# Kernel tuning notes

Measured on AMD Instinct MI355X. Metric: run time of the kernel, lower is better.

The kernel has to match this reference:

```python
import jax, jax.numpy as jnp
import numpy as np

EPS = 1e-05

def _rmsnorm(h, w, eps=EPS):
    var = jnp.mean(h * h, axis=-1, keepdims=True)
    return h * jax.lax.rsqrt(var + eps) * w

def setup_inputs() -> dict:
    key = jax.random.key(0)
    ks = jax.random.split(key, 9)
    B, S, H, I, R = 2, 4096, 4096, 14336, 1592
    s_h = 1.0 / np.sqrt(H)
    s_r = 1.0 / np.sqrt(R)
    s_i = 1.0 / np.sqrt(I)
    return {
        "x": jax.random.normal(ks[0], (B, S, H), jnp.float32),
        "residual": jax.random.normal(ks[1], (B, S, H), jnp.float32),
        "ln_w": jnp.ones((H,), jnp.float32),
        "w_gate_v": jax.random.normal(ks[2], (H, R), jnp.float32) * s_h,
        "w_gate_u": jax.random.normal(ks[3], (R, I), jnp.float32) * s_r,
        "w_up_v": jax.random.normal(ks[4], (H, R), jnp.float32) * s_h,
        "w_up_u": jax.random.normal(ks[5], (R, I), jnp.float32) * s_r,
        "w_down_v": jax.random.normal(ks[6], (I, R), jnp.float32) * s_i,
        "w_down_u": jax.random.normal(ks[7], (R, H), jnp.float32) * s_r,
    }

def reference(x, residual, ln_w, w_gate_v, w_gate_u, w_up_v, w_up_u, w_down_v, w_down_u):
    # fused residual add + RMSNorm (as in the fused NKI kernel path)
    h = x + residual                    # [B,S,H]
    n = _rmsnorm(h, ln_w)               # [B,S,H]
    # low-rank gate / up projections: H -> R -> I
    gate = jax.nn.silu(jnp.einsum('bsh,hr,ri->bsi', n, w_gate_v, w_gate_u))
    up = jnp.einsum('bsh,hr,ri->bsi', n, w_up_v, w_up_u)
    # low-rank down projection: I -> R -> H
    out = jnp.einsum('bsi,ir,rh->bsh', gate * up, w_down_v, w_down_u)
    return out
```

## Files before the change

### kernel.cpp

```cpp
#include <hip/hip_runtime.h>
#include <cstdint>
#include <cstddef>

typedef __attribute__((ext_vector_type(8))) short short8;
typedef __attribute__((ext_vector_type(4))) float floatx4;

__device__ __forceinline__ float bf2f(unsigned short u) {
    union { float f; uint32_t i; } v; v.i = ((uint32_t)u) << 16; return v.f;
}
__device__ __forceinline__ unsigned short f2bf(float f) {
    union { float f; uint32_t i; } v; v.f = f;
    uint32_t r = v.i + 0x7FFFu + ((v.i >> 16) & 1u);
    return (unsigned short)(r >> 16);
}

__device__ __forceinline__ void gl_lds16(const unsigned short* g, unsigned short* l) {
    __builtin_amdgcn_global_load_lds(
        (const __attribute__((address_space(1))) unsigned int*)g,
        (__attribute__((address_space(3))) unsigned int*)l,
        16, 0, 0);
}

__device__ __forceinline__ int xcd_swizzle(int bid, int nwg) {
    const int nx = 8;
    const int q = nwg / nx, r = nwg % nx;
    const int xcd = bid % nx, local = bid / nx;
    return (xcd < r ? xcd * (q + 1) : r * (q + 1) + (xcd - r) * q) + local;
}

__global__ __launch_bounds__(256)
void add_rmsnorm_kernel(const float* __restrict__ x, const float* __restrict__ res,
                        const float* __restrict__ w, unsigned short* __restrict__ out,
                        int H, float invH)
{
    const size_t row = blockIdx.x;
    const float4* xv = (const float4*)(x + row * (size_t)H);
    const float4* rv = (const float4*)(res + row * (size_t)H);
    const float4* wv = (const float4*)w;
    const int nvec = H >> 2;
    float4 h[8];
    float s = 0.f;
    int cnt = 0;
    for (int idx = threadIdx.x; idx < nvec; idx += 256) {
        float4 a = xv[idx], b = rv[idx];
        float4 hh = make_float4(a.x + b.x, a.y + b.y, a.z + b.z, a.w + b.w);
        h[cnt++] = hh;
        s += hh.x * hh.x + hh.y * hh.y + hh.z * hh.z + hh.w * hh.w;
    }
    __shared__ float red[256];
    red[threadIdx.x] = s;
    __syncthreads();
    for (int off = 128; off > 0; off >>= 1) {
        if (threadIdx.x < off) red[threadIdx.x] += red[threadIdx.x + off];
        __syncthreads();
    }
    const float scale = rsqrtf(red[0] * invH + 1e-5f);
    ushort4* ov = (ushort4*)(out + row * (size_t)H);
    cnt = 0;
    for (int idx = threadIdx.x; idx < nvec; idx += 256) {
        float4 hh = h[cnt++];
        float4 ww = wv[idx];
        ushort4 o;
        o.x = f2bf(hh.x * scale * ww.x);
        o.y = f2bf(hh.y * scale * ww.y);
        o.z = f2bf(hh.z * scale * ww.z);
        o.w = f2bf(hh.w * scale * ww.w);
        ov[idx] = o;
    }
}

__global__ __launch_bounds__(256)
void transpose_cast(const float* __restrict__ src, unsigned short* __restrict__ dst,
                    int P, int Q, int Pld, int Qld)
{
    __shared__ float tile[32][33];
    const int qt = blockIdx.x * 32, pt = blockIdx.y * 32;
    const int tx = threadIdx.x, ty = threadIdx.y;
    #pragma unroll
    for (int r = 0; r < 32; r += 8) {
        int p = pt + ty + r, q = qt + tx;
        tile[ty + r][tx] = (p < P && q < Q) ? src[(size_t)p * Q + q] : 0.f;
    }
    __syncthreads();
    #pragma unroll
    for (int r = 0; r < 32; r += 8) {
        int q = qt + ty + r, p = pt + tx;
        if (q < Qld && p < Pld) dst[(size_t)q * Pld + p] = f2bf(tile[tx][ty + r]);
    }
}

template<int EPI>
__global__ __launch_bounds__(256)
void gemm128(const unsigned short* __restrict__ A,
             const unsigned short* __restrict__ Bt,
             void* __restrict__ Cv,
             const unsigned short* __restrict__ other,
             int N, int Nld, int K, int gx)
{
    __shared__ unsigned short As[128 * 32];
    __shared__ unsigned short Bs[128 * 32];
    const int tid  = threadIdx.x;
    const int bid  = xcd_swizzle(blockIdx.x, gridDim.x);
    const int n0   = (bid % gx) << 7;
    const int m0   = (bid / gx) << 7;
    const int lane = tid & 63;
    const int wave = tid >> 6;
    const int quad = lane >> 4;
    const int lr   = lane & 15;
    const int wm   = (wave >> 1) << 6;
    const int wn   = (wave & 1) << 6;

    const floatx4 zero = {0.f, 0.f, 0.f, 0.f};
    floatx4 acc[4][4];
    #pragma unroll
    for (int i = 0; i < 4; i++)
        #pragma unroll
        for (int j = 0; j < 4; j++) acc[i][j] = zero;

    const int lrow = lane >> 2;
    const int lk8  = (lane & 3) << 3;

    unsigned short* lA0 = As + (wave * 32) * 32;
    unsigned short* lA1 = lA0 + 16 * 32;
    unsigned short* lB0 = Bs + (wave * 32) * 32;
    unsigned short* lB1 = lB0 + 16 * 32;

    const unsigned short* gA0 = A + (size_t)(m0 + wave * 32 + lrow) * K + lk8;
    const unsigned short* gA1 = gA0 + (size_t)16 * K;
    int rb0 = n0 + wave * 32 + lrow;      if (rb0 >= Nld) rb0 = 0;
    int rb1 = n0 + wave * 32 + 16 + lrow; if (rb1 >= Nld) rb1 = 0;
    const unsigned short* gB0 = Bt + (size_t)rb0 * K + lk8;
    const unsigned short* gB1 = Bt + (size_t)rb1 * K + lk8;

    for (int k0 = 0; k0 < K; k0 += 32) {
        gl_lds16(gA0 + k0, lA0);
        gl_lds16(gA1 + k0, lA1);
        gl_lds16(gB0 + k0, lB0);
        gl_lds16(gB1 + k0, lB1);
        __syncthreads();

        short8 af[4], bfr[4];
        #pragma unroll
        for (int mi = 0; mi < 4; mi++)
            af[mi] = *(const short8*)(As + (wm + mi * 16 + lr) * 32 + quad * 8);
        #pragma unroll
        for (int ni = 0; ni < 4; ni++)
            bfr[ni] = *(const short8*)(Bs + (wn + ni * 16 + lr) * 32 + quad * 8);
        #pragma unroll
        for (int mi = 0; mi < 4; mi++)
            #pragma unroll
            for (int ni = 0; ni < 4; ni++)
                acc[mi][ni] = __builtin_amdgcn_mfma_f32_16x16x32_bf16(
                    af[mi], bfr[ni], acc[mi][ni], 0, 0, 0);
        __syncthreads();
    }

    #pragma unroll
    for (int mi = 0; mi < 4; mi++) {
        const int growb = m0 + wm + mi * 16 + quad * 4;
        #pragma unroll
        for (int ni = 0; ni < 4; ni++) {
            const int col = n0 + wn + ni * 16 + lr;
            if (col < Nld) {
                #pragma unroll
                for (int i = 0; i < 4; i++) {
                    const size_t idx = (size_t)(growb + i) * Nld + col;
                    const float v = acc[mi][ni][i];
                    if (EPI == 0) {
                        ((unsigned short*)Cv)[idx] = (col < N) ? f2bf(v) : (unsigned short)0;
                    } else if (EPI == 1) {
                        ((float*)Cv)[idx] = v;
                    } else {
                        const float o = bf2f(other[idx]);
                        const float sg = v / (1.f + __expf(-v));
                        ((unsigned short*)Cv)[idx] = f2bf(sg * o);
                    }
                }
            }
        }
    }
}

extern "C" void kernel_launch(void* const* d_in, const int* in_sizes, int n_in,
                              void* d_out, int out_size, void* d_ws, size_t ws_size,
                              hipStream_t stream)
{
    const float* x   = (const float*)d_in[0];
    const float* res = (const float*)d_in[1];
    const float* lnw = (const float*)d_in[2];
    const float* wgv = (const float*)d_in[3];
    const float* wgu = (const float*)d_in[4];
    const float* wuv = (const float*)d_in[5];
    const float* wuu = (const float*)d_in[6];
    const float* wdv = (const float*)d_in[7];
    const float* wdu = (const float*)d_in[8];

    const int H = in_sizes[2];
    const int T = (int)((long long)in_sizes[0] / H);
    const int R = in_sizes[3] / H;
    const int I = in_sizes[4] / R;
    const int Rp = (R + 63) & ~63;

    unsigned short* p = (unsigned short*)d_ws;
    unsigned short* Wgv_t = p; p += (size_t)Rp * H;
    unsigned short* Wuv_t = p; p += (size_t)Rp * H;
    unsigned short* Wgu_t = p; p += (size_t)I * Rp;
    unsigned short* Wuu_t = p; p += (size_t)I * Rp;
    unsigned short* Wdv_t = p; p += (size_t)Rp * I;
    unsigned short* Wdu_t = p; p += (size_t)H * Rp;
    unsigned short* nbuf  = p; p += (size_t)T * H;
    unsigned short* g1    = p; p += (size_t)T * Rp;
    unsigned short* u1    = p; p += (size_t)T * Rp;
    unsigned short* upm   = p; p += (size_t)T * I;
    unsigned short* d1    = nbuf;

    dim3 tb(32, 8);
    transpose_cast<<<dim3((Rp + 31) / 32, (H + 31) / 32), tb, 0, stream>>>(wgv, Wgv_t, H, R, H, Rp);
    transpose_cast<<<dim3((Rp + 31) / 32, (H + 31) / 32), tb, 0, stream>>>(wuv, Wuv_t, H, R, H, Rp);
    transpose_cast<<<dim3((I + 31) / 32, (Rp + 31) / 32), tb, 0, stream>>>(wgu, Wgu_t, R, I, Rp, I);
    transpose_cast<<<dim3((I + 31) / 32, (Rp + 31) / 32), tb, 0, stream>>>(wuu, Wuu_t, R, I, Rp, I);
    transpose_cast<<<dim3((Rp + 31) / 32, (I + 31) / 32), tb, 0, stream>>>(wdv, Wdv_t, I, R, I, Rp);
    transpose_cast<<<dim3((H + 31) / 32, (Rp + 31) / 32), tb, 0, stream>>>(wdu, Wdu_t, R, H, Rp, H);

    add_rmsnorm_kernel<<<T, 256, 0, stream>>>(x, res, lnw, nbuf, H, 1.0f / (float)H);

    const int gxR = (Rp + 127) / 128;
    const int gxI = (I + 127) / 128;
    const int gxH = (H + 127) / 128;
    const int gy  = T / 128;

    gemm128<0><<<gxR * gy, 256, 0, stream>>>(nbuf, Wgv_t, g1, nullptr, R, Rp, H, gxR);
    gemm128<0><<<gxR * gy, 256, 0, stream>>>(nbuf, Wuv_t, u1, nullptr, R, Rp, H, gxR);
    gemm128<0><<<gxI * gy, 256, 0, stream>>>(u1, Wuu_t, upm, nullptr, I, I, Rp, gxI);
    gemm128<2><<<gxI * gy, 256, 0, stream>>>(g1, Wgu_t, upm, upm, I, I, Rp, gxI);
    gemm128<0><<<gxR * gy, 256, 0, stream>>>(upm, Wdv_t, d1, nullptr, R, Rp, I, gxR);
    gemm128<1><<<gxH * gy, 256, 0, stream>>>(d1, Wdu_t, d_out, nullptr, H, H, Rp, gxH);
}
```

Measured before the change: 3.081 ms.

## Double-buffer LDS tiles in GEMM and merge gate/up down-rank projections

The GEMM k-loop now ping-pongs between two LDS buffers. Global-to-LDS loads for the next K tile are issued before the MFMAs on the current tile, so load latency can overlap compute. The gate and up H->R projections become one GEMM over the concatenated transposed weights, written into a shared [T, 2Rp] buffer. The next GEMMs read from it through a separate lda. A launch-bounds occupancy hint of 4 blocks is added, and the padded-column zero check is dropped because the padded weights are already zero. LDS use doubles per block, which may limit occupancy.

```diff
diff --git a/kernel.cpp b/kernel.cpp
--- a/kernel.cpp
+++ b/kernel.cpp
@@ -90,15 +90,17 @@
 }
 
 template<int EPI>
-__global__ __launch_bounds__(256)
+__global__ __launch_bounds__(256, 4)
 void gemm128(const unsigned short* __restrict__ A,
              const unsigned short* __restrict__ Bt,
              void* __restrict__ Cv,
              const unsigned short* __restrict__ other,
-             int N, int Nld, int K, int gx)
-{
-    __shared__ unsigned short As[128 * 32];
-    __shared__ unsigned short Bs[128 * 32];
+             int Nld, int K, int lda, int gx)
+{
+    __shared__ unsigned short As0[128 * 32];
+    __shared__ unsigned short As1[128 * 32];
+    __shared__ unsigned short Bs0[128 * 32];
+    __shared__ unsigned short Bs1[128 * 32];
     const int tid  = threadIdx.x;
     const int bid  = xcd_swizzle(blockIdx.x, gridDim.x);
     const int n0   = (bid % gx) << 7;
@@ -119,41 +121,59 @@
 
     const int lrow = lane >> 2;
     const int lk8  = (lane & 3) << 3;
-
-    unsigned short* lA0 = As + (wave * 32) * 32;
-    unsigned short* lA1 = lA0 + 16 * 32;
-    unsigned short* lB0 = Bs + (wave * 32) * 32;
-    unsigned short* lB1 = lB0 + 16 * 32;
-
-    const unsigned short* gA0 = A + (size_t)(m0 + wave * 32 + lrow) * K + lk8;
-    const unsigned short* gA1 = gA0 + (size_t)16 * K;
+    const int woff = wave * 1024;
+
+    const unsigned short* gA0 = A + (size_t)(m0 + wave * 32 + lrow) * lda + lk8;
+    const unsigned short* gA1 = gA0 + (size_t)16 * lda;
     int rb0 = n0 + wave * 32 + lrow;      if (rb0 >= Nld) rb0 = 0;
     int rb1 = n0 + wave * 32 + 16 + lrow; if (rb1 >= Nld) rb1 = 0;
     const unsigned short* gB0 = Bt + (size_t)rb0 * K + lk8;
     const unsigned short* gB1 = Bt + (size_t)rb1 * K + lk8;
 
-    for (int k0 = 0; k0 < K; k0 += 32) {
-        gl_lds16(gA0 + k0, lA0);
-        gl_lds16(gA1 + k0, lA1);
-        gl_lds16(gB0 + k0, lB0);
-        gl_lds16(gB1 + k0, lB1);
+#define STAGE(ASL, BSL, kk)                          \
+    {                                                \
+        gl_lds16(gA0 + (kk), (ASL) + woff);          \
+        gl_lds16(gA1 + (kk), (ASL) + woff + 512);    \
+        gl_lds16(gB0 + (kk), (BSL) + woff);          \
+        gl_lds16(gB1 + (kk), (BSL) + woff + 512);    \
+    }
+
+#define COMPUTE(ASL, BSL)                                                          \
+    {                                                                              \
+        short8 af[4], bfr[4];                                                      \
+        _Pragma("unroll")                                                          \
+        for (int mi = 0; mi < 4; mi++)                                             \
+            af[mi] = *(const short8*)((ASL) + (wm + mi * 16 + lr) * 32 + quad * 8);\
+        _Pragma("unroll")                                                          \
+        for (int ni = 0; ni < 4; ni++)                                             \
+            bfr[ni] = *(const short8*)((BSL) + (wn + ni * 16 + lr) * 32 + quad * 8);\
+        _Pragma("unroll")                                                          \
+        for (int mi = 0; mi < 4; mi++)                                             \
+            _Pragma("unroll")                                                      \
+            for (int ni = 0; ni < 4; ni++)                                         \
+                acc[mi][ni] = __builtin_amdgcn_mfma_f32_16x16x32_bf16(             \
+                    af[mi], bfr[ni], acc[mi][ni], 0, 0, 0);                        \
+    }
+
+    STAGE(As0, Bs0, 0);
+    __syncthreads();
+    int k0 = 0;
+    for (;;) {
+        int kn = k0 + 32;
+        if (kn < K) STAGE(As1, Bs1, kn);
+        COMPUTE(As0, Bs0);
         __syncthreads();
-
-        short8 af[4], bfr[4];
-        #pragma unroll
-        for (int mi = 0; mi < 4; mi++)
-            af[mi] = *(const short8*)(As + (wm + mi * 16 + lr) * 32 + quad * 8);
-        #pragma unroll
-        for (int ni = 0; ni < 4; ni++)
-            bfr[ni] = *(const short8*)(Bs + (wn + ni * 16 + lr) * 32 + quad * 8);
-        #pragma unroll
-        for (int mi = 0; mi < 4; mi++)
-            #pragma unroll
-            for (int ni = 0; ni < 4; ni++)
-                acc[mi][ni] = __builtin_amdgcn_mfma_f32_16x16x32_bf16(
-                    af[mi], bfr[ni], acc[mi][ni], 0, 0, 0);
+        k0 = kn;
+        if (k0 >= K) break;
+        kn = k0 + 32;
+        if (kn < K) STAGE(As0, Bs0, kn);
+        COMPUTE(As1, Bs1);
         __syncthreads();
-    }
+        k0 = kn;
+        if (k0 >= K) break;
+    }
+#undef STAGE
+#undef COMPUTE
 
     #pragma unroll
     for (int mi = 0; mi < 4; mi++) {
@@ -167,7 +187,7 @@
                     const size_t idx = (size_t)(growb + i) * Nld + col;
                     const float v = acc[mi][ni][i];
                     if (EPI == 0) {
-                        ((unsigned short*)Cv)[idx] = (col < N) ? f2bf(v) : (unsigned short)0;
+                        ((unsigned short*)Cv)[idx] = f2bf(v);
                     } else if (EPI == 1) {
                         ((float*)Cv)[idx] = v;
                     } else {
@@ -200,6 +220,7 @@
     const int R = in_sizes[3] / H;
     const int I = in_sizes[4] / R;
     const int Rp = (R + 63) & ~63;
+    const int R2 = 2 * Rp;
 
     unsigned short* p = (unsigned short*)d_ws;
     unsigned short* Wgv_t = p; p += (size_t)Rp * H;
@@ -209,8 +230,7 @@
     unsigned short* Wdv_t = p; p += (size_t)Rp * I;
     unsigned short* Wdu_t = p; p += (size_t)H * Rp;
     unsigned short* nbuf  = p; p += (size_t)T * H;
-    unsigned short* g1    = p; p += (size_t)T * Rp;
-    unsigned short* u1    = p; p += (size_t)T * Rp;
+    unsigned short* gu1   = p; p += (size_t)T * R2;
     unsigned short* upm   = p; p += (size_t)T * I;
     unsigned short* d1    = nbuf;
 
@@ -224,15 +244,15 @@
 
     add_rmsnorm_kernel<<<T, 256, 0, stream>>>(x, res, lnw, nbuf, H, 1.0f / (float)H);
 
-    const int gxR = (Rp + 127) / 128;
-    const int gxI = (I + 127) / 128;
-    const int gxH = (H + 127) / 128;
-    const int gy  = T / 128;
-
-    gemm128<0><<<gxR * gy, 256, 0, stream>>>(nbuf, Wgv_t, g1, nullptr, R, Rp, H, gxR);
-    gemm128<0><<<gxR * gy, 256, 0, stream>>>(nbuf, Wuv_t, u1, nullptr, R, Rp, H, gxR);
-    gemm128<0><<<gxI * gy, 256, 0, stream>>>(u1, Wuu_t, upm, nullptr, I, I, Rp, gxI);
-    gemm128<2><<<gxI * gy, 256, 0, stream>>>(g1, Wgu_t, upm, upm, I, I, Rp, gxI);
-    gemm128<0><<<gxR * gy, 256, 0, stream>>>(upm, Wdv_t, d1, nullptr, R, Rp, I, gxR);
-    gemm128<1><<<gxH * gy, 256, 0, stream>>>(d1, Wdu_t, d_out, nullptr, H, H, Rp, gxH);
-}
+    const int gx12 = R2 / 128;
+    const int gxR  = (Rp + 127) / 128;
+    const int gxI  = (I + 127) / 128;
+    const int gxH  = (H + 127) / 128;
+    const int gy   = T / 128;
+
+    gemm128<0><<<gx12 * gy, 256, 0, stream>>>(nbuf, Wgv_t, gu1, nullptr, R2, H, H, gx12);
+    gemm128<0><<<gxI * gy, 256, 0, stream>>>(gu1 + Rp, Wuu_t, upm, nullptr, I, Rp, R2, gxI);
+    gemm128<2><<<gxI * gy, 256, 0, stream>>>(gu1, Wgu_t, upm, upm, I, Rp, R2, gxI);
+    gemm128<0><<<gxR * gy, 256, 0, stream>>>(upm, Wdv_t, d1, nullptr, Rp, I, I, gxR);
+    gemm128<1><<<gxH * gy, 256, 0, stream>>>(d1, Wdu_t, d_out, nullptr, H, Rp, Rp, gxH);
+}
```

Result: faster. 2.705 ms (-12.2%).
